# Kernel optimization log

Measured on AMD Instinct MI355X. Metric: run time of the kernel, lower is better.

The kernel has to match this reference:

```python
import jax, jax.numpy as jnp
import numpy as np
import math

D_MODEL = 96
D_STATE = 16
D_CONV = 3
EXPAND = 2
D_INNER = EXPAND * D_MODEL          # 192
DT_RANK = math.ceil(D_MODEL / 16)   # 6
B_SZ, H_SZ, W_SZ = 2, 56, 56


def setup_inputs() -> dict:
    key = jax.random.key(0)
    ks = jax.random.split(key, 10)
    x = jax.random.normal(ks[0], (B_SZ, H_SZ, W_SZ, D_MODEL), jnp.float32)
    W_in = jax.random.normal(ks[1], (D_MODEL, 2 * D_INNER), jnp.float32) * 0.02
    conv_w = jax.random.normal(ks[2], (D_CONV, D_CONV, 1, D_INNER), jnp.float32) * 0.1
    conv_b = jax.random.normal(ks[3], (D_INNER,), jnp.float32) * 0.02
    W_xproj = jax.random.normal(ks[4], (D_INNER, DT_RANK + 2 * D_STATE), jnp.float32) * 0.02
    dt_std = DT_RANK ** -0.5
    W_dt = jax.random.uniform(ks[5], (DT_RANK, D_INNER), jnp.float32, -dt_std, dt_std)
    # dt_proj bias init: inverse-softplus of dt ~ LogUniform(dt_min, dt_max)
    dt_min, dt_max = 1e-3, 1e-1
    dt = jnp.exp(jax.random.uniform(ks[6], (D_INNER,), jnp.float32)
                 * (math.log(dt_max) - math.log(dt_min)) + math.log(dt_min))
    dt = jnp.clip(dt, 1e-4, None)
    b_dt = dt + jnp.log(-jnp.expm1(-dt))
    # A_log initialized to broadcast arange(1..d_state) (as in the source, no log taken)
    A_log = jnp.tile(jnp.arange(1, D_STATE + 1, dtype=jnp.float32)[None, :], (D_INNER, 1))
    D_skip = jnp.ones((D_INNER,), jnp.float32)
    W_out = jax.random.normal(ks[7], (D_INNER, D_MODEL), jnp.float32) * 0.02
    return {"x": x, "W_in": W_in, "conv_w": conv_w, "conv_b": conv_b,
            "W_xproj": W_xproj, "W_dt": W_dt, "b_dt": b_dt,
            "A_log": A_log, "D_skip": D_skip, "W_out": W_out}


def _selective_scan(xs, dt, A, Bm, Cm, D_skip):
    """Canonical Mamba selective scan.
    xs, dt: (G, L, C); Bm, Cm: (G, L, N); A: (C, N); D_skip: (C,).
    h_l = exp(dt_l * A) * h_{l-1} + dt_l * B_l * x_l ;  y_l = <h_l, C_l> + D * x_l
    """
    dA = jnp.exp(dt[..., None] * A)                              # (G,L,C,N)
    dBx = dt[..., None] * Bm[:, :, None, :] * xs[..., None]      # (G,L,C,N)

    def step(h, inp):
        dA_l, dBx_l, C_l = inp                                   # (G,C,N),(G,C,N),(G,N)
        h = dA_l * h + dBx_l
        y = jnp.einsum('gcn,gn->gc', h, C_l)
        return h, y

    G, L, C = xs.shape
    h0 = jnp.zeros((G, C, D_STATE), xs.dtype)
    _, ys = jax.lax.scan(step, h0, (jnp.moveaxis(dA, 1, 0),
                                    jnp.moveaxis(dBx, 1, 0),
                                    jnp.moveaxis(Cm, 1, 0)))
    ys = jnp.moveaxis(ys, 0, 1)                                  # (G,L,C)
    return ys + D_skip * xs


def reference(x, W_in, conv_w, conv_b, W_xproj, W_dt, b_dt, A_log, D_skip, W_out):
    B, H, W, _ = x.shape  # H == W required (source sums transposed scans directly)
    xz = x @ W_in                                                # (B,H,W,2*d_inner)
    xm, z = jnp.split(xz, 2, axis=-1)
    pad = (D_CONV - 1) // 2
    xm = jax.lax.conv_general_dilated(
        xm, conv_w, (1, 1), [(pad, pad), (pad, pad)],
        dimension_numbers=('NHWC', 'HWIO', 'NHWC'),
        feature_group_count=D_INNER) + conv_b                    # depthwise conv
    # 4 scan directions
    xt = jnp.swapaxes(xm, 1, 2)
    xs4 = jnp.stack([xm, jnp.flip(xm, 2), xt, jnp.flip(xt, 1)], 0)  # (4,B,H,W,C)
    G, L = 4 * B, H * W
    xs = xs4.reshape(G, L, D_INNER)
    x_dbl = xs @ W_xproj                                          # (G,L,dt_rank+2N)
    dtr, Bm, Cm = jnp.split(x_dbl, [DT_RANK, DT_RANK + D_STATE], axis=-1)
    dt = jax.nn.softplus(dtr @ W_dt + b_dt)                       # (G,L,d_inner)
    A = -jnp.exp(A_log)                                           # (d_inner, N)
    ys = _selective_scan(xs, dt, A, Bm, Cm, D_skip)               # (G,L,d_inner)
    y = ys.reshape(4, B, H, W, D_INNER).sum(0)                    # sum 4 directions
    y = jax.nn.silu(z) * y
    return y @ W_out                                              # (B,H,W,d_model)
```

## Files before the change

kernel.cpp:

```cpp
#include <hip/hip_runtime.h>
#include <math.h>

#define NPIX 6272
#define LVAL 3136
#define CIN 192
#define NST 16
#define HW 56

__device__ __forceinline__ float softplusf(float v) {
    return (v > 20.0f) ? v : log1pf(expf(v));
}

__device__ __forceinline__ void dir_geom(int d, int b, int& si, int& sj, int& off) {
    if (d == 0)      { si = HW;  sj = 1;   off = b * LVAL; }
    else if (d == 1) { si = HW;  sj = -1;  off = b * LVAL + (HW - 1); }
    else if (d == 2) { si = 1;   sj = HW;  off = b * LVAL; }
    else             { si = -1;  sj = HW;  off = b * LVAL + (HW - 1); }
}

__global__ __launch_bounds__(384) void k_inproj(
    const float* __restrict__ x, const float* __restrict__ W_in,
    float* __restrict__ xm, float* __restrict__ z)
{
    __shared__ __align__(16) float xs[96][20];
    const int p0 = blockIdx.x * 16;
    const int t = threadIdx.x;
    for (int e = t; e < 16 * 96; e += 384) {
        int p = e / 96, kk = e % 96;
        xs[kk][p] = x[p0 * 96 + e];
    }
    __syncthreads();
    float acc[16];
#pragma unroll
    for (int p = 0; p < 16; ++p) acc[p] = 0.f;
    for (int k = 0; k < 96; ++k) {
        float w = W_in[k * 384 + t];
        float4 x0 = *(const float4*)&xs[k][0];
        float4 x1 = *(const float4*)&xs[k][4];
        float4 x2 = *(const float4*)&xs[k][8];
        float4 x3 = *(const float4*)&xs[k][12];
        acc[0]  = fmaf(x0.x, w, acc[0]);  acc[1]  = fmaf(x0.y, w, acc[1]);
        acc[2]  = fmaf(x0.z, w, acc[2]);  acc[3]  = fmaf(x0.w, w, acc[3]);
        acc[4]  = fmaf(x1.x, w, acc[4]);  acc[5]  = fmaf(x1.y, w, acc[5]);
        acc[6]  = fmaf(x1.z, w, acc[6]);  acc[7]  = fmaf(x1.w, w, acc[7]);
        acc[8]  = fmaf(x2.x, w, acc[8]);  acc[9]  = fmaf(x2.y, w, acc[9]);
        acc[10] = fmaf(x2.z, w, acc[10]); acc[11] = fmaf(x2.w, w, acc[11]);
        acc[12] = fmaf(x3.x, w, acc[12]); acc[13] = fmaf(x3.y, w, acc[13]);
        acc[14] = fmaf(x3.z, w, acc[14]); acc[15] = fmaf(x3.w, w, acc[15]);
    }
#pragma unroll
    for (int p = 0; p < 16; ++p) {
        int pix = p0 + p;
        if (t < 192) xm[pix * CIN + t] = acc[p];
        else         z[pix * CIN + (t - 192)] = acc[p];
    }
}

__global__ __launch_bounds__(256) void k_conv(
    const float* __restrict__ xm, const float* __restrict__ cw,
    const float* __restrict__ cb, float* __restrict__ xcv)
{
    int e = blockIdx.x * 256 + threadIdx.x;
    if (e >= NPIX * (CIN / 4)) return;
    int cq = (e % (CIN / 4)) * 4;
    int pix = e / (CIN / 4);
    int w = pix % HW;
    int rest = pix / HW;
    int h = rest % HW;
    int b = rest / HW;
    float4 acc = *(const float4*)&cb[cq];
#pragma unroll
    for (int ky = 0; ky < 3; ++ky) {
        int hh = h + ky - 1;
        if (hh < 0 || hh >= HW) continue;
#pragma unroll
        for (int kx = 0; kx < 3; ++kx) {
            int ww = w + kx - 1;
            if (ww < 0 || ww >= HW) continue;
            float4 xv = *(const float4*)&xm[((b * HW + hh) * HW + ww) * CIN + cq];
            float4 wv = *(const float4*)&cw[(ky * 3 + kx) * CIN + cq];
            acc.x = fmaf(xv.x, wv.x, acc.x);
            acc.y = fmaf(xv.y, wv.y, acc.y);
            acc.z = fmaf(xv.z, wv.z, acc.z);
            acc.w = fmaf(xv.w, wv.w, acc.w);
        }
    }
    *(float4*)&xcv[pix * CIN + cq] = acc;
}

__global__ __launch_bounds__(512) void k_xproj_dt(
    const float* __restrict__ xcv, const float* __restrict__ W_xproj,
    const float* __restrict__ W_dt, const float* __restrict__ b_dt,
    float* __restrict__ Bp, float* __restrict__ Cp, float2* __restrict__ dtx2)
{
    __shared__ __align__(16) float xs[192][28];
    __shared__ float part[2][24][40];
    __shared__ float dtr_lds[24][8];
    const int p0 = blockIdx.x * 24;
    const int t = threadIdx.x;
    for (int e = t; e < 24 * 192; e += 512) {
        int p = e / 192, kk = e % 192;
        int pix = p0 + p;
        xs[kk][p] = (pix < NPIX) ? xcv[pix * CIN + kk] : 0.f;
    }
    __syncthreads();
    const int th = t & 255;
    const int kh = t >> 8;
    const int j  = th % 40;
    const int pq = th / 40;
    if (pq < 6) {
        const int jc = (j < 38) ? j : 37;
        float a0 = 0.f, a1 = 0.f, a2 = 0.f, a3 = 0.f;
        const int k0 = kh * 96;
        for (int k = k0; k < k0 + 96; ++k) {
            float w = W_xproj[k * 38 + jc];
            float4 xv = *(const float4*)&xs[k][pq * 4];
            a0 = fmaf(xv.x, w, a0); a1 = fmaf(xv.y, w, a1);
            a2 = fmaf(xv.z, w, a2); a3 = fmaf(xv.w, w, a3);
        }
        part[kh][pq * 4 + 0][j] = a0;
        part[kh][pq * 4 + 1][j] = a1;
        part[kh][pq * 4 + 2][j] = a2;
        part[kh][pq * 4 + 3][j] = a3;
    }
    __syncthreads();
    if (kh == 0 && pq < 6 && j < 38) {
#pragma unroll
        for (int q = 0; q < 4; ++q) {
            int p = pq * 4 + q;
            float r = part[0][p][j] + part[1][p][j];
            int pix = p0 + p;
            if (j < 6) dtr_lds[p][j] = r;
            if (pix < NPIX) {
                if (j < 6)       ;
                else if (j < 22) Bp[pix * NST + (j - 6)] = r;
                else             Cp[pix * NST + (j - 22)] = r;
            }
        }
    }
    __syncthreads();
    for (int e = t; e < 24 * 192; e += 512) {
        int p = e / 192, c = e % 192;
        int pix = p0 + p;
        if (pix >= NPIX) continue;
        float v = b_dt[c];
#pragma unroll
        for (int r = 0; r < 6; ++r)
            v = fmaf(dtr_lds[p][r], W_dt[r * CIN + c], v);
        dtx2[(size_t)pix * CIN + c] = make_float2(softplusf(v), xs[c][p]);
    }
}

template<int CHUNK>
__global__ __launch_bounds__(384) void k_scan_p1(
    const float2* __restrict__ dtx2, const float* __restrict__ Bp,
    const float* __restrict__ A_log,
    float* __restrict__ Pbuf, float* __restrict__ qbuf)
{
    constexpr int CPR = HW / CHUNK;
    __shared__ __align__(16) float Bs[CHUNK * NST];
    const int g = blockIdx.y;
    const int k = blockIdx.x;
    const int t = threadIdx.x;
    const int wv = t >> 6;
    const int lane = t & 63;
    const int cl = lane & 31, nh = lane >> 5;
    const int c = wv * 32 + cl;
    const int n0 = nh * 8;
    const int d = g >> 1, b = g & 1;
    int si, sj, off;
    dir_geom(d, b, si, sj, off);
    const int base = off + (k / CPR) * si + ((k % CPR) * CHUNK) * sj;

    for (int e = t; e < CHUNK * NST; e += 384) {
        int jj = e >> 4, n = e & 15;
        Bs[e] = Bp[(base + jj * sj) * NST + n];
    }

    const float LOG2E = 1.4426950408889634f;
    float a2[8];
    {
        const float4* Ar = (const float4*)(A_log + c * NST + n0);
#pragma unroll
        for (int q = 0; q < 2; ++q) {
            float4 v = Ar[q];
            a2[q*4+0] = -expf(v.x) * LOG2E;
            a2[q*4+1] = -expf(v.y) * LOG2E;
            a2[q*4+2] = -expf(v.z) * LOG2E;
            a2[q*4+3] = -expf(v.w) * LOG2E;
        }
    }
    __syncthreads();

    float h[8];
#pragma unroll
    for (int i = 0; i < 8; ++i) h[i] = 0.f;
    float Sdt = 0.f;

    float2 dv = dtx2[(size_t)base * CIN + c];
    for (int jj = 0; jj < CHUNK; ++jj) {
        float dt_c = dv.x, x_c = dv.y;
        int jn = (jj + 1 < CHUNK) ? jj + 1 : jj;
        dv = dtx2[(size_t)(base + jn * sj) * CIN + c];
        float dtx = dt_c * x_c;
        Sdt += dt_c;
        float Bv[8];
        {
            const float4* Brow = (const float4*)(Bs + jj * NST + n0);
            float4 t0 = Brow[0], t1 = Brow[1];
            Bv[0]=t0.x; Bv[1]=t0.y; Bv[2]=t0.z; Bv[3]=t0.w;
            Bv[4]=t1.x; Bv[5]=t1.y; Bv[6]=t1.z; Bv[7]=t1.w;
        }
#pragma unroll
        for (int i = 0; i < 8; ++i) {
            float dA = exp2f(dt_c * a2[i]);
            h[i] = fmaf(dA, h[i], dtx * Bv[i]);
        }
    }
    float P[8];
#pragma unroll
    for (int i = 0; i < 8; ++i) P[i] = exp2f(a2[i] * Sdt);

    float4* Pd = (float4*)(Pbuf + ((size_t)(k * 8 + g) * CIN + c) * NST + n0);
    float4* qd = (float4*)(qbuf + ((size_t)(k * 8 + g) * CIN + c) * NST + n0);
    Pd[0] = make_float4(P[0], P[1], P[2], P[3]);
    Pd[1] = make_float4(P[4], P[5], P[6], P[7]);
    qd[0] = make_float4(h[0], h[1], h[2], h[3]);
    qd[1] = make_float4(h[4], h[5], h[6], h[7]);
}

__global__ __launch_bounds__(256) void k_scan_fix(
    const float* __restrict__ Pbuf, float* __restrict__ qbuf, int nch)
{
    const int g = blockIdx.y;
    const int lo = blockIdx.x * 256 + threadIdx.x;
    const size_t stride = (size_t)8 * CIN * NST;
    size_t idx  = (size_t)g * CIN * NST + lo;
    size_t pidx = idx;
    float Pr[8], qr[8];
#pragma unroll
    for (int i = 0; i < 8; ++i) { Pr[i] = Pbuf[pidx]; qr[i] = qbuf[pidx]; pidx += stride; }
    float h = 0.f;
    for (int k = 0; k < nch; k += 8) {
        float Pn[8], qn[8];
        if (k + 8 < nch) {
#pragma unroll
            for (int i = 0; i < 8; ++i) {
                Pn[i] = Pbuf[pidx + (size_t)i * stride];
                qn[i] = qbuf[pidx + (size_t)i * stride];
            }
        } else {
#pragma unroll
            for (int i = 0; i < 8; ++i) { Pn[i] = 0.f; qn[i] = 0.f; }
        }
#pragma unroll
        for (int i = 0; i < 8; ++i) {
            qbuf[idx] = h;
            h = fmaf(Pr[i], h, qr[i]);
            idx += stride;
        }
#pragma unroll
        for (int i = 0; i < 8; ++i) { Pr[i] = Pn[i]; qr[i] = qn[i]; }
        pidx += (size_t)8 * stride;
    }
}

template<int CHUNK>
__global__ __launch_bounds__(384) void k_scan_p2(
    const float2* __restrict__ dtx2, const float* __restrict__ Bp,
    const float* __restrict__ Cp, const float* __restrict__ A_log,
    const float* __restrict__ D_skip,
    const float* __restrict__ qbuf, float* __restrict__ Y4)
{
    constexpr int CPR = HW / CHUNK;
    __shared__ __align__(16) float Bs[CHUNK * NST];
    __shared__ __align__(16) float Cs[CHUNK * NST];
    const int g = blockIdx.y;
    const int k = blockIdx.x;
    const int t = threadIdx.x;
    const int wv = t >> 6;
    const int lane = t & 63;
    const int cl = lane & 31, nh = lane >> 5;
    const int c = wv * 32 + cl;
    const int n0 = nh * 8;
    const int d = g >> 1, b = g & 1;
    int si, sj, off;
    dir_geom(d, b, si, sj, off);
    const int base = off + (k / CPR) * si + ((k % CPR) * CHUNK) * sj;

    for (int e = t; e < CHUNK * NST; e += 384) {
        int jj = e >> 4, n = e & 15;
        int pa = (base + jj * sj) * NST + n;
        Bs[e] = Bp[pa];
        Cs[e] = Cp[pa];
    }

    const float LOG2E = 1.4426950408889634f;
    float a2[8];
    {
        const float4* Ar = (const float4*)(A_log + c * NST + n0);
#pragma unroll
        for (int q = 0; q < 2; ++q) {
            float4 v = Ar[q];
            a2[q*4+0] = -expf(v.x) * LOG2E;
            a2[q*4+1] = -expf(v.y) * LOG2E;
            a2[q*4+2] = -expf(v.z) * LOG2E;
            a2[q*4+3] = -expf(v.w) * LOG2E;
        }
    }
    const float Dc = D_skip[c];

    float h[8];
    {
        const float4* qd = (const float4*)(qbuf + ((size_t)(k * 8 + g) * CIN + c) * NST + n0);
        float4 v0 = qd[0], v1 = qd[1];
        h[0]=v0.x; h[1]=v0.y; h[2]=v0.z; h[3]=v0.w;
        h[4]=v1.x; h[5]=v1.y; h[6]=v1.z; h[7]=v1.w;
    }
    __syncthreads();

    float* yo = Y4 + ((size_t)d * NPIX + (size_t)b * LVAL + (size_t)k * CHUNK) * CIN;

    float2 dv = dtx2[(size_t)base * CIN + c];
    for (int jj = 0; jj < CHUNK; ++jj) {
        float dt_c = dv.x, x_c = dv.y;
        int jn = (jj + 1 < CHUNK) ? jj + 1 : jj;
        dv = dtx2[(size_t)(base + jn * sj) * CIN + c];
        float dtx = dt_c * x_c;
        float Bv[8], Cv[8];
        {
            const float4* Brow = (const float4*)(Bs + jj * NST + n0);
            const float4* Crow = (const float4*)(Cs + jj * NST + n0);
            float4 t0 = Brow[0], t1 = Brow[1];
            float4 u0 = Crow[0], u1 = Crow[1];
            Bv[0]=t0.x; Bv[1]=t0.y; Bv[2]=t0.z; Bv[3]=t0.w;
            Bv[4]=t1.x; Bv[5]=t1.y; Bv[6]=t1.z; Bv[7]=t1.w;
            Cv[0]=u0.x; Cv[1]=u0.y; Cv[2]=u0.z; Cv[3]=u0.w;
            Cv[4]=u1.x; Cv[5]=u1.y; Cv[6]=u1.z; Cv[7]=u1.w;
        }
        float yc0 = 0.f, yc1 = 0.f;
#pragma unroll
        for (int i = 0; i < 8; i += 2) {
            float dA0 = exp2f(dt_c * a2[i]);
            float dA1 = exp2f(dt_c * a2[i+1]);
            h[i]   = fmaf(dA0, h[i],   dtx * Bv[i]);
            h[i+1] = fmaf(dA1, h[i+1], dtx * Bv[i+1]);
            yc0 = fmaf(h[i],   Cv[i],   yc0);
            yc1 = fmaf(h[i+1], Cv[i+1], yc1);
        }
        float yc = yc0 + yc1;
        yc += __shfl_xor(yc, 32, 64);
        if (nh == 0)
            yo[jj * CIN + c] = fmaf(Dc, x_c, yc);
    }
}

__global__ __launch_bounds__(384) void k_gateout(
    const float* __restrict__ Y4, const float* __restrict__ z,
    const float* __restrict__ W_out, float* __restrict__ out)
{
    __shared__ __align__(16) float xs[192][20];
    const int p0 = blockIdx.x * 16;
    const int t = threadIdx.x;
    const size_t NP = (size_t)NPIX * CIN;
    for (int e = t; e < 16 * 192; e += 384) {
        int p = e / 192, c = e % 192;
        size_t idx = (size_t)(p0 + p) * CIN + c;
        float s = Y4[idx] + Y4[idx + NP] + Y4[idx + 2 * NP] + Y4[idx + 3 * NP];
        float zz = z[idx];
        float sig = 1.f / (1.f + expf(-zz));
        xs[c][p] = zz * sig * s;
    }
    __syncthreads();
    const int j  = t % 96;
    const int ph = t / 96;
    float acc[4] = {0.f, 0.f, 0.f, 0.f};
    for (int k = 0; k < 192; ++k) {
        float w = W_out[k * 96 + j];
        float4 xv = *(const float4*)&xs[k][ph * 4];
        acc[0] = fmaf(xv.x, w, acc[0]); acc[1] = fmaf(xv.y, w, acc[1]);
        acc[2] = fmaf(xv.z, w, acc[2]); acc[3] = fmaf(xv.w, w, acc[3]);
    }
#pragma unroll
    for (int p = 0; p < 4; ++p)
        out[(p0 + ph * 4 + p) * 96 + j] = acc[p];
}

template<int CHUNK>
static void launch_scan(const float2* dtx2, const float* Bp, const float* Cp,
                        const float* A_log, const float* D_skip,
                        float* Pbuf, float* qbuf, float* Y4, hipStream_t stream)
{
    const int nch = LVAL / CHUNK;
    k_scan_p1<CHUNK><<<dim3(nch, 8), 384, 0, stream>>>(dtx2, Bp, A_log, Pbuf, qbuf);
    k_scan_fix<<<dim3(12, 8), 256, 0, stream>>>(Pbuf, qbuf, nch);
    k_scan_p2<CHUNK><<<dim3(nch, 8), 384, 0, stream>>>(dtx2, Bp, Cp, A_log, D_skip, qbuf, Y4);
}

extern "C" void kernel_launch(void* const* d_in, const int* in_sizes, int n_in,
                              void* d_out, int out_size, void* d_ws, size_t ws_size,
                              hipStream_t stream) {
    const float* x      = (const float*)d_in[0];
    const float* W_in   = (const float*)d_in[1];
    const float* conv_w = (const float*)d_in[2];
    const float* conv_b = (const float*)d_in[3];
    const float* W_xproj= (const float*)d_in[4];
    const float* W_dt   = (const float*)d_in[5];
    const float* b_dt   = (const float*)d_in[6];
    const float* A_log  = (const float*)d_in[7];
    const float* D_skip = (const float*)d_in[8];
    const float* W_out  = (const float*)d_in[9];
    float* out = (float*)d_out;

    float* ws   = (float*)d_ws;
    float* xm   = ws;
    float* z    = xm  + NPIX * CIN;
    float* xcv  = z   + NPIX * CIN;
    float2* dtx2= (float2*)(xcv + NPIX * CIN);
    float* Bp   = (float*)(dtx2 + (size_t)NPIX * CIN);
    float* Cp   = Bp  + NPIX * NST;
    float* Y4   = Cp  + NPIX * NST;
    float* Pbuf = Y4  + (size_t)4 * NPIX * CIN;

    const size_t base_fl = 11038720;
    const size_t ws_fl = ws_size / 4;
    int chunk;
    if (ws_fl >= base_fl + (size_t)2 * 112 * 24576) chunk = 28;
    else                                            chunk = 56;
    float* qbuf = Pbuf + (size_t)(LVAL / chunk) * 8 * CIN * NST;

    k_inproj  <<<NPIX / 16, 384, 0, stream>>>(x, W_in, xm, z);
    k_conv    <<<(NPIX * (CIN / 4)) / 256, 256, 0, stream>>>(xm, conv_w, conv_b, xcv);
    k_xproj_dt<<<(NPIX + 23) / 24, 512, 0, stream>>>(xcv, W_xproj, W_dt, b_dt, Bp, Cp, dtx2);
    if (chunk == 28) launch_scan<28>(dtx2, Bp, Cp, A_log, D_skip, Pbuf, qbuf, Y4, stream);
    else             launch_scan<56>(dtx2, Bp, Cp, A_log, D_skip, Pbuf, qbuf, Y4, stream);
    k_gateout <<<NPIX / 16, 384, 0, stream>>>(Y4, z, W_out, out);
}
```

Baseline: 197.0 us.

## Fuse depthwise conv into xproj and merge scan passes into one cooperative kernel

```diff
diff --git a/kernel.cpp b/kernel.cpp
--- a/kernel.cpp
+++ b/kernel.cpp
@@ -1,4 +1,5 @@
 #include <hip/hip_runtime.h>
+#include <hip/hip_cooperative_groups.h>
 #include <math.h>
 
 #define NPIX 6272
@@ -56,40 +57,10 @@
     }
 }
 
-__global__ __launch_bounds__(256) void k_conv(
+__global__ __launch_bounds__(512) void k_xproj_dt(
     const float* __restrict__ xm, const float* __restrict__ cw,
-    const float* __restrict__ cb, float* __restrict__ xcv)
-{
-    int e = blockIdx.x * 256 + threadIdx.x;
-    if (e >= NPIX * (CIN / 4)) return;
-    int cq = (e % (CIN / 4)) * 4;
-    int pix = e / (CIN / 4);
-    int w = pix % HW;
-    int rest = pix / HW;
-    int h = rest % HW;
-    int b = rest / HW;
-    float4 acc = *(const float4*)&cb[cq];
-#pragma unroll
-    for (int ky = 0; ky < 3; ++ky) {
-        int hh = h + ky - 1;
-        if (hh < 0 || hh >= HW) continue;
-#pragma unroll
-        for (int kx = 0; kx < 3; ++kx) {
-            int ww = w + kx - 1;
-            if (ww < 0 || ww >= HW) continue;
-            float4 xv = *(const float4*)&xm[((b * HW + hh) * HW + ww) * CIN + cq];
-            float4 wv = *(const float4*)&cw[(ky * 3 + kx) * CIN + cq];
-            acc.x = fmaf(xv.x, wv.x, acc.x);
-            acc.y = fmaf(xv.y, wv.y, acc.y);
-            acc.z = fmaf(xv.z, wv.z, acc.z);
-            acc.w = fmaf(xv.w, wv.w, acc.w);
-        }
-    }
-    *(float4*)&xcv[pix * CIN + cq] = acc;
-}
-
-__global__ __launch_bounds__(512) void k_xproj_dt(
-    const float* __restrict__ xcv, const float* __restrict__ W_xproj,
+    const float* __restrict__ cb,
+    const float* __restrict__ W_xproj,
     const float* __restrict__ W_dt, const float* __restrict__ b_dt,
     float* __restrict__ Bp, float* __restrict__ Cp, float2* __restrict__ dtx2)
 {
@@ -101,7 +72,27 @@
     for (int e = t; e < 24 * 192; e += 512) {
         int p = e / 192, kk = e % 192;
         int pix = p0 + p;
-        xs[kk][p] = (pix < NPIX) ? xcv[pix * CIN + kk] : 0.f;
+        float v = 0.f;
+        if (pix < NPIX) {
+            int w = pix % HW;
+            int rest = pix / HW;
+            int h = rest % HW;
+            int b = rest / HW;
+            v = cb[kk];
+#pragma unroll
+            for (int ky = 0; ky < 3; ++ky) {
+                int hh = h + ky - 1;
+                if (hh < 0 || hh >= HW) continue;
+#pragma unroll
+                for (int kx = 0; kx < 3; ++kx) {
+                    int ww = w + kx - 1;
+                    if (ww < 0 || ww >= HW) continue;
+                    v = fmaf(xm[((b * HW + hh) * HW + ww) * CIN + kk],
+                             cw[(ky * 3 + kx) * CIN + kk], v);
+                }
+            }
+        }
+        xs[kk][p] = v;
     }
     __syncthreads();
     const int th = t & 255;
@@ -152,15 +143,20 @@
 }
 
 template<int CHUNK>
-__global__ __launch_bounds__(384) void k_scan_p1(
+__global__ __launch_bounds__(384, 6) void k_scan_coop(
     const float2* __restrict__ dtx2, const float* __restrict__ Bp,
-    const float* __restrict__ A_log,
-    float* __restrict__ Pbuf, float* __restrict__ qbuf)
+    const float* __restrict__ Cp, const float* __restrict__ A_log,
+    const float* __restrict__ D_skip,
+    float* __restrict__ Pbuf, float* __restrict__ qbuf,
+    float* __restrict__ Y4)
 {
     constexpr int CPR = HW / CHUNK;
+    constexpr int NCH = LVAL / CHUNK;
     __shared__ __align__(16) float Bs[CHUNK * NST];
-    const int g = blockIdx.y;
-    const int k = blockIdx.x;
+    __shared__ __align__(16) float Cs[CHUNK * NST];
+    const int bid = blockIdx.x;
+    const int k = bid % NCH;
+    const int g = bid / NCH;
     const int t = threadIdx.x;
     const int wv = t >> 6;
     const int lane = t & 63;
@@ -174,7 +170,9 @@
 
     for (int e = t; e < CHUNK * NST; e += 384) {
         int jj = e >> 4, n = e & 15;
-        Bs[e] = Bp[(base + jj * sj) * NST + n];
+        int pa = (base + jj * sj) * NST + n;
+        Bs[e] = Bp[pa];
+        Cs[e] = Cp[pa];
     }
 
     const float LOG2E = 1.4426950408889634f;
@@ -192,41 +190,180 @@
     }
     __syncthreads();
 
+    const float2* dp = dtx2 + (size_t)base * CIN + c;
+    const ptrdiff_t dstep = (ptrdiff_t)sj * CIN;
+
     float h[8];
 #pragma unroll
     for (int i = 0; i < 8; ++i) h[i] = 0.f;
     float Sdt = 0.f;
-
-    float2 dv = dtx2[(size_t)base * CIN + c];
+    {
+        float2 dv = dp[0];
+        for (int jj = 0; jj < CHUNK; ++jj) {
+            float dt_c = dv.x, x_c = dv.y;
+            int jn = (jj + 1 < CHUNK) ? jj + 1 : jj;
+            dv = dp[(ptrdiff_t)jn * dstep];
+            float dtx = dt_c * x_c;
+            Sdt += dt_c;
+            float4 t0 = *(const float4*)(Bs + jj * NST + n0);
+            float4 t1 = *(const float4*)(Bs + jj * NST + n0 + 4);
+            float Bv[8] = {t0.x,t0.y,t0.z,t0.w,t1.x,t1.y,t1.z,t1.w};
+#pragma unroll
+            for (int i = 0; i < 8; ++i) {
+                float dA = exp2f(dt_c * a2[i]);
+                h[i] = fmaf(dA, h[i], dtx * Bv[i]);
+            }
+        }
+    }
+    {
+        float4* Pd = (float4*)(Pbuf + ((size_t)(k * 8 + g) * CIN + c) * NST + n0);
+        float4* qd = (float4*)(qbuf + ((size_t)(k * 8 + g) * CIN + c) * NST + n0);
+        float P0 = exp2f(a2[0] * Sdt), P1 = exp2f(a2[1] * Sdt);
+        float P2 = exp2f(a2[2] * Sdt), P3 = exp2f(a2[3] * Sdt);
+        float P4 = exp2f(a2[4] * Sdt), P5 = exp2f(a2[5] * Sdt);
+        float P6 = exp2f(a2[6] * Sdt), P7 = exp2f(a2[7] * Sdt);
+        Pd[0] = make_float4(P0, P1, P2, P3);
+        Pd[1] = make_float4(P4, P5, P6, P7);
+        qd[0] = make_float4(h[0], h[1], h[2], h[3]);
+        qd[1] = make_float4(h[4], h[5], h[6], h[7]);
+    }
+
+    cooperative_groups::this_grid().sync();
+
+    {
+        const int gtid = bid * 384 + t;
+        if (gtid < 8 * CIN * NST) {
+            const int gg = gtid / (CIN * NST);
+            const int lo = gtid % (CIN * NST);
+            const size_t stride = (size_t)8 * CIN * NST;
+            size_t idx  = (size_t)gg * CIN * NST + lo;
+            size_t pidx = idx;
+            float Pr[8], qr[8];
+#pragma unroll
+            for (int i = 0; i < 8; ++i) { Pr[i] = Pbuf[pidx]; qr[i] = qbuf[pidx]; pidx += stride; }
+            float hh = 0.f;
+            for (int kk = 0; kk < NCH; kk += 8) {
+                float Pn[8], qn[8];
+                if (kk + 8 < NCH) {
+#pragma unroll
+                    for (int i = 0; i < 8; ++i) {
+                        Pn[i] = Pbuf[pidx + (size_t)i * stride];
+                        qn[i] = qbuf[pidx + (size_t)i * stride];
+                    }
+                } else {
+#pragma unroll
+                    for (int i = 0; i < 8; ++i) { Pn[i] = 0.f; qn[i] = 0.f; }
+                }
+#pragma unroll
+                for (int i = 0; i < 8; ++i) {
+                    qbuf[idx] = hh;
+                    hh = fmaf(Pr[i], hh, qr[i]);
+                    idx += stride;
+                }
+#pragma unroll
+                for (int i = 0; i < 8; ++i) { Pr[i] = Pn[i]; qr[i] = qn[i]; }
+                pidx += (size_t)8 * stride;
+            }
+        }
+    }
+
+    cooperative_groups::this_grid().sync();
+
+    {
+        const float4* qd = (const float4*)(qbuf + ((size_t)(k * 8 + g) * CIN + c) * NST + n0);
+        float4 v0q = qd[0], v1q = qd[1];
+        h[0]=v0q.x; h[1]=v0q.y; h[2]=v0q.z; h[3]=v0q.w;
+        h[4]=v1q.x; h[5]=v1q.y; h[6]=v1q.z; h[7]=v1q.w;
+    }
+    const float Dc = D_skip[c];
+    float* yo = Y4 + ((size_t)d * NPIX + (size_t)b * LVAL + (size_t)k * CHUNK) * CIN;
+    {
+        float2 dv = dp[0];
+        for (int jj = 0; jj < CHUNK; ++jj) {
+            float dt_c = dv.x, x_c = dv.y;
+            int jn = (jj + 1 < CHUNK) ? jj + 1 : jj;
+            dv = dp[(ptrdiff_t)jn * dstep];
+            float dtx = dt_c * x_c;
+            float4 t0 = *(const float4*)(Bs + jj * NST + n0);
+            float4 t1 = *(const float4*)(Bs + jj * NST + n0 + 4);
+            float4 u0 = *(const float4*)(Cs + jj * NST + n0);
+            float4 u1 = *(const float4*)(Cs + jj * NST + n0 + 4);
+            float Bv[8] = {t0.x,t0.y,t0.z,t0.w,t1.x,t1.y,t1.z,t1.w};
+            float Cv[8] = {u0.x,u0.y,u0.z,u0.w,u1.x,u1.y,u1.z,u1.w};
+            float yc0 = 0.f, yc1 = 0.f;
+#pragma unroll
+            for (int i = 0; i < 8; i += 2) {
+                float dA0 = exp2f(dt_c * a2[i]);
+                float dA1 = exp2f(dt_c * a2[i+1]);
+                h[i]   = fmaf(dA0, h[i],   dtx * Bv[i]);
+                h[i+1] = fmaf(dA1, h[i+1], dtx * Bv[i+1]);
+                yc0 = fmaf(h[i],   Cv[i],   yc0);
+                yc1 = fmaf(h[i+1], Cv[i+1], yc1);
+            }
+            float yc = yc0 + yc1;
+            yc += __shfl_xor(yc, 32, 64);
+            if (nh == 0)
+                yo[jj * CIN + c] = fmaf(Dc, x_c, yc);
+        }
+    }
+}
+
+template<int CHUNK>
+__global__ __launch_bounds__(384) void k_scan_p1(
+    const float2* __restrict__ dtx2, const float* __restrict__ Bp,
+    const float* __restrict__ A_log,
+    float* __restrict__ Pbuf, float* __restrict__ qbuf)
+{
+    constexpr int CPR = HW / CHUNK;
+    __shared__ __align__(16) float Bs[CHUNK * NST];
+    const int g = blockIdx.y;
+    const int k = blockIdx.x;
+    const int ch = blockIdx.z;
+    const int t = threadIdx.x;
+    const int wv = t >> 6;
+    const int lane = t & 63;
+    const int cl = lane & 15, nh = lane >> 4;
+    const int c = ch * 96 + wv * 16 + cl;
+    const int n0 = nh * 4;
+    const int d = g >> 1, b = g & 1;
+    int si, sj, off;
+    dir_geom(d, b, si, sj, off);
+    const int base = off + (k / CPR) * si + ((k % CPR) * CHUNK) * sj;
+
+    for (int e = t; e < CHUNK * NST; e += 384) {
+        int jj = e >> 4, n = e & 15;
+        Bs[e] = Bp[(base + jj * sj) * NST + n];
+    }
+    const float LOG2E = 1.4426950408889634f;
+    float a2[4];
+    {
+        float4 v = *(const float4*)(A_log + c * NST + n0);
+        a2[0] = -expf(v.x) * LOG2E; a2[1] = -expf(v.y) * LOG2E;
+        a2[2] = -expf(v.z) * LOG2E; a2[3] = -expf(v.w) * LOG2E;
+    }
+    __syncthreads();
+    float h[4] = {0.f, 0.f, 0.f, 0.f};
+    float Sdt = 0.f;
+    const float2* dp = dtx2 + (size_t)base * CIN + c;
+    const ptrdiff_t dstep = (ptrdiff_t)sj * CIN;
+    float2 dv = dp[0];
     for (int jj = 0; jj < CHUNK; ++jj) {
         float dt_c = dv.x, x_c = dv.y;
         int jn = (jj + 1 < CHUNK) ? jj + 1 : jj;
-        dv = dtx2[(size_t)(base + jn * sj) * CIN + c];
+        dv = dp[(ptrdiff_t)jn * dstep];
         float dtx = dt_c * x_c;
         Sdt += dt_c;
-        float Bv[8];
-        {
-            const float4* Brow = (const float4*)(Bs + jj * NST + n0);
-            float4 t0 = Brow[0], t1 = Brow[1];
-            Bv[0]=t0.x; Bv[1]=t0.y; Bv[2]=t0.z; Bv[3]=t0.w;
-            Bv[4]=t1.x; Bv[5]=t1.y; Bv[6]=t1.z; Bv[7]=t1.w;
-        }
-#pragma unroll
-        for (int i = 0; i < 8; ++i) {
+        float4 t0 = *(const float4*)(Bs + jj * NST + n0);
+#pragma unroll
+        for (int i = 0; i < 4; ++i) {
             float dA = exp2f(dt_c * a2[i]);
-            h[i] = fmaf(dA, h[i], dtx * Bv[i]);
-        }
-    }
-    float P[8];
-#pragma unroll
-    for (int i = 0; i < 8; ++i) P[i] = exp2f(a2[i] * Sdt);
-
+            h[i] = fmaf(dA, h[i], (&t0.x)[i] * dtx);
+        }
+    }
     float4* Pd = (float4*)(Pbuf + ((size_t)(k * 8 + g) * CIN + c) * NST + n0);
     float4* qd = (float4*)(qbuf + ((size_t)(k * 8 + g) * CIN + c) * NST + n0);
-    Pd[0] = make_float4(P[0], P[1], P[2], P[3]);
-    Pd[1] = make_float4(P[4], P[5], P[6], P[7]);
+    Pd[0] = make_float4(exp2f(a2[0]*Sdt), exp2f(a2[1]*Sdt), exp2f(a2[2]*Sdt), exp2f(a2[3]*Sdt));
     qd[0] = make_float4(h[0], h[1], h[2], h[3]);
-    qd[1] = make_float4(h[4], h[5], h[6], h[7]);
 }
 
 __global__ __launch_bounds__(256) void k_scan_fix(
@@ -277,12 +414,13 @@
     __shared__ __align__(16) float Cs[CHUNK * NST];
     const int g = blockIdx.y;
     const int k = blockIdx.x;
+    const int ch = blockIdx.z;
     const int t = threadIdx.x;
     const int wv = t >> 6;
     const int lane = t & 63;
-    const int cl = lane & 31, nh = lane >> 5;
-    const int c = wv * 32 + cl;
-    const int n0 = nh * 8;
+    const int cl = lane & 15, nh = lane >> 4;
+    const int c = ch * 96 + wv * 16 + cl;
+    const int n0 = nh * 4;
     const int d = g >> 1, b = g & 1;
     int si, sj, off;
     dir_geom(d, b, si, sj, off);
@@ -294,61 +432,39 @@
         Bs[e] = Bp[pa];
         Cs[e] = Cp[pa];
     }
-
     const float LOG2E = 1.4426950408889634f;
-    float a2[8];
-    {
-        const float4* Ar = (const float4*)(A_log + c * NST + n0);
-#pragma unroll
-        for (int q = 0; q < 2; ++q) {
-            float4 v = Ar[q];
-            a2[q*4+0] = -expf(v.x) * LOG2E;
-            a2[q*4+1] = -expf(v.y) * LOG2E;
-            a2[q*4+2] = -expf(v.z) * LOG2E;
-            a2[q*4+3] = -expf(v.w) * LOG2E;
-        }
+    float a2[4];
+    {
+        float4 v = *(const float4*)(A_log + c * NST + n0);
+        a2[0] = -expf(v.x) * LOG2E; a2[1] = -expf(v.y) * LOG2E;
+        a2[2] = -expf(v.z) * LOG2E; a2[3] = -expf(v.w) * LOG2E;
     }
     const float Dc = D_skip[c];
-
-    float h[8];
-    {
-        const float4* qd = (const float4*)(qbuf + ((size_t)(k * 8 + g) * CIN + c) * NST + n0);
-        float4 v0 = qd[0], v1 = qd[1];
-        h[0]=v0.x; h[1]=v0.y; h[2]=v0.z; h[3]=v0.w;
-        h[4]=v1.x; h[5]=v1.y; h[6]=v1.z; h[7]=v1.w;
-    }
-    __syncthreads();
-
+    float h[4];
+    {
+        float4 v0q = *(const float4*)(qbuf + ((size_t)(k * 8 + g) * CIN + c) * NST + n0);
+        h[0]=v0q.x; h[1]=v0q.y; h[2]=v0q.z; h[3]=v0q.w;
+    }
+    __syncthreads();
     float* yo = Y4 + ((size_t)d * NPIX + (size_t)b * LVAL + (size_t)k * CHUNK) * CIN;
-
-    float2 dv = dtx2[(size_t)base * CIN + c];
+    const float2* dp = dtx2 + (size_t)base * CIN + c;
+    const ptrdiff_t dstep = (ptrdiff_t)sj * CIN;
+    float2 dv = dp[0];
     for (int jj = 0; jj < CHUNK; ++jj) {
         float dt_c = dv.x, x_c = dv.y;
         int jn = (jj + 1 < CHUNK) ? jj + 1 : jj;
-        dv = dtx2[(size_t)(base + jn * sj) * CIN + c];
+        dv = dp[(ptrdiff_t)jn * dstep];
         float dtx = dt_c * x_c;
-        float Bv[8], Cv[8];
-        {
-            const float4* Brow = (const float4*)(Bs + jj * NST + n0);
-            const float4* Crow = (const float4*)(Cs + jj * NST + n0);
-            float4 t0 = Brow[0], t1 = Brow[1];
-            float4 u0 = Crow[0], u1 = Crow[1];
-            Bv[0]=t0.x; Bv[1]=t0.y; Bv[2]=t0.z; Bv[3]=t0.w;
-            Bv[4]=t1.x; Bv[5]=t1.y; Bv[6]=t1.z; Bv[7]=t1.w;
-            Cv[0]=u0.x; Cv[1]=u0.y; Cv[2]=u0.z; Cv[3]=u0.w;
-            Cv[4]=u1.x; Cv[5]=u1.y; Cv[6]=u1.z; Cv[7]=u1.w;
-        }
-        float yc0 = 0.f, yc1 = 0.f;
-#pragma unroll
-        for (int i = 0; i < 8; i += 2) {
-            float dA0 = exp2f(dt_c * a2[i]);
-            float dA1 = exp2f(dt_c * a2[i+1]);
-            h[i]   = fmaf(dA0, h[i],   dtx * Bv[i]);
-            h[i+1] = fmaf(dA1, h[i+1], dtx * Bv[i+1]);
-            yc0 = fmaf(h[i],   Cv[i],   yc0);
-            yc1 = fmaf(h[i+1], Cv[i+1], yc1);
-        }
-        float yc = yc0 + yc1;
+        float4 t0 = *(const float4*)(Bs + jj * NST + n0);
+        float4 u0 = *(const float4*)(Cs + jj * NST + n0);
+        float yc = 0.f;
+#pragma unroll
+        for (int i = 0; i < 4; ++i) {
+            float dA = exp2f(dt_c * a2[i]);
+            h[i] = fmaf(dA, h[i], (&t0.x)[i] * dtx);
+            yc = fmaf(h[i], (&u0.x)[i], yc);
+        }
+        yc += __shfl_xor(yc, 16, 64);
         yc += __shfl_xor(yc, 32, 64);
         if (nh == 0)
             yo[jj * CIN + c] = fmaf(Dc, x_c, yc);
@@ -384,17 +500,6 @@
 #pragma unroll
     for (int p = 0; p < 4; ++p)
         out[(p0 + ph * 4 + p) * 96 + j] = acc[p];
-}
-
-template<int CHUNK>
-static void launch_scan(const float2* dtx2, const float* Bp, const float* Cp,
-                        const float* A_log, const float* D_skip,
-                        float* Pbuf, float* qbuf, float* Y4, hipStream_t stream)
-{
-    const int nch = LVAL / CHUNK;
-    k_scan_p1<CHUNK><<<dim3(nch, 8), 384, 0, stream>>>(dtx2, Bp, A_log, Pbuf, qbuf);
-    k_scan_fix<<<dim3(12, 8), 256, 0, stream>>>(Pbuf, qbuf, nch);
-    k_scan_p2<CHUNK><<<dim3(nch, 8), 384, 0, stream>>>(dtx2, Bp, Cp, A_log, D_skip, qbuf, Y4);
 }
 
 extern "C" void kernel_launch(void* const* d_in, const int* in_sizes, int n_in,
@@ -430,9 +535,37 @@
     float* qbuf = Pbuf + (size_t)(LVAL / chunk) * 8 * CIN * NST;
 
     k_inproj  <<<NPIX / 16, 384, 0, stream>>>(x, W_in, xm, z);
-    k_conv    <<<(NPIX * (CIN / 4)) / 256, 256, 0, stream>>>(xm, conv_w, conv_b, xcv);
-    k_xproj_dt<<<(NPIX + 23) / 24, 512, 0, stream>>>(xcv, W_xproj, W_dt, b_dt, Bp, Cp, dtx2);
-    if (chunk == 28) launch_scan<28>(dtx2, Bp, Cp, A_log, D_skip, Pbuf, qbuf, Y4, stream);
-    else             launch_scan<56>(dtx2, Bp, Cp, A_log, D_skip, Pbuf, qbuf, Y4, stream);
+    k_xproj_dt<<<(NPIX + 23) / 24, 512, 0, stream>>>(xm, conv_w, conv_b,
+                                                     W_xproj, W_dt, b_dt, Bp, Cp, dtx2);
+
+    {
+        const float2* a_dtx2 = dtx2;
+        const float* a_Bp = Bp; const float* a_Cp = Cp;
+        const float* a_A = A_log; const float* a_D = D_skip;
+        float* a_P = Pbuf; float* a_q = qbuf; float* a_Y = Y4;
+        void* kargs[8] = { (void*)&a_dtx2, (void*)&a_Bp, (void*)&a_Cp,
+                           (void*)&a_A, (void*)&a_D, (void*)&a_P,
+                           (void*)&a_q, (void*)&a_Y };
+        hipError_t cerr;
+        if (chunk == 28)
+            cerr = hipLaunchCooperativeKernel((void*)k_scan_coop<28>,
+                     dim3(8 * (LVAL / 28)), dim3(384), kargs, 0, stream);
+        else
+            cerr = hipLaunchCooperativeKernel((void*)k_scan_coop<56>,
+                     dim3(8 * (LVAL / 56)), dim3(384), kargs, 0, stream);
+        if (cerr != hipSuccess) {
+            const int nch = LVAL / chunk;
+            if (chunk == 28) {
+                k_scan_p1<28><<<dim3(nch, 8, 2), 384, 0, stream>>>(dtx2, Bp, A_log, Pbuf, qbuf);
+                k_scan_fix<<<dim3(12, 8), 256, 0, stream>>>(Pbuf, qbuf, nch);
+                k_scan_p2<28><<<dim3(nch, 8, 2), 384, 0, stream>>>(dtx2, Bp, Cp, A_log, D_skip, qbuf, Y4);
+            } else {
+                k_scan_p1<56><<<dim3(nch, 8, 2), 384, 0, stream>>>(dtx2, Bp, A_log, Pbuf, qbuf);
+                k_scan_fix<<<dim3(12, 8), 256, 0, stream>>>(Pbuf, qbuf, nch);
+                k_scan_p2<56><<<dim3(nch, 8, 2), 384, 0, stream>>>(dtx2, Bp, Cp, A_log, D_skip, qbuf, Y4);
+            }
+        }
+    }
+
     k_gateout <<<NPIX / 16, 384, 0, stream>>>(Y4, z, W_out, out);
 }
```

Result: slower. 430.1 us (+118.4%).
